# Optimization experiments

Measured on AMD Instinct MI355X. Metric: run time of the kernel, lower is better.

## Reference

```python
import jax, jax.numpy as jnp
import numpy as np
import math

L = 16.0
DT = 1.0
TAU = 10.0
THRESHOLD = 1.0
ALPHA = 0.01
DECAY = math.exp(-DT / TAU)

@jax.custom_vjp
def multibit_spike(x):
    # forward: floor(x) clipped to [0, L]
    return jnp.clip(jnp.floor(x), 0.0, L)

def _spike_fwd(x):
    return multibit_spike(x), x

def _spike_bwd(x, g):
    dist = jnp.abs(x - jnp.round(x))
    scale = jnp.clip(1.0 - 2.0 * dist, 0.0, 1.0)
    in_range = ((x >= 0.0) & (x <= L + 1.0)).astype(g.dtype)
    return (g * in_range * scale,)

multibit_spike.defvjp(_spike_fwd, _spike_bwd)

def setup_inputs() -> dict:
    key = jax.random.key(0)
    k_x, k_w = jax.random.split(key)
    B, T, IN, H = 16, 2048, 512, 512
    # SNN-aware init: std = 0.5*threshold / (sqrt(fan_in)*0.3)
    std = 0.5 * THRESHOLD / (math.sqrt(IN) * 0.3)
    x = jax.random.normal(k_x, (B, T, IN), dtype=jnp.float32)
    W = jax.random.normal(k_w, (H, IN), dtype=jnp.float32) * std
    b = jnp.zeros((H,), dtype=jnp.float32)
    return {"x": x, "W": W, "b": b}

def reference(x, W, b):
    B, T, _ = x.shape
    Hd = W.shape[0]
    # batched linear projection of the whole sequence (compute-heavy GEMM)
    h = jnp.einsum('bti,hi->bth', x, W) + b  # [B, T, H]
    v0 = jnp.zeros((B, Hd), dtype=x.dtype)
    theta0 = jnp.full((B, Hd), THRESHOLD, dtype=x.dtype)

    def step(carry, i_t):
        v, theta = carry
        v = v * DECAY + i_t
        clamp_limit = L * theta * 2.0
        v = jnp.clip(v, -clamp_limit, clamp_limit)
        spike = multibit_spike(v / theta)
        v = v - spike * theta
        theta = theta + ALPHA * spike - ALPHA * (theta - THRESHOLD)
        return (v, theta), spike

    (v_f, theta_f), spikes_tbh = jax.lax.scan(step, (v0, theta0), jnp.swapaxes(h, 0, 1))
    spikes = jnp.swapaxes(spikes_tbh, 0, 1)  # [B, T, H]
    return spikes, v_f, theta_f
```

## Files before the change

kernel.cpp:

```cpp
#include <hip/hip_runtime.h>

#define B_  16
#define T_  2048
#define IN_ 512
#define H_  512
#define M_  (B_ * T_)

#define BM 128
#define BN 128
#define BK 16
#define LDT (BM + 4)

static __device__ __forceinline__ float4 ld4(const float* p) {
    return *reinterpret_cast<const float4*>(p);
}

__global__ __launch_bounds__(256)
void gemm_xwT(const float* __restrict__ X, const float* __restrict__ W,
              const float* __restrict__ bias, float* __restrict__ Hout) {
    __shared__ float As[BK][LDT];
    __shared__ float Bs[BK][LDT];

    const int tid = threadIdx.x;
    const int m0  = blockIdx.x * BM;
    const int n0  = blockIdx.y * BN;

    const int tx = tid & 15;
    const int ty = tid >> 4;

    const int row = tid >> 2;
    const int kph = (tid & 3) * 4;

    const float* pa0 = X + (size_t)(m0 + row) * IN_ + kph;
    const float* pa1 = pa0 + (size_t)64 * IN_;
    const float* pb0 = W + (size_t)(n0 + row) * IN_ + kph;
    const float* pb1 = pb0 + (size_t)64 * IN_;

    float4 ra0 = ld4(pa0), ra1 = ld4(pa1), rb0 = ld4(pb0), rb1 = ld4(pb1);

    float acc[8][8];
#pragma unroll
    for (int i = 0; i < 8; ++i)
#pragma unroll
        for (int j = 0; j < 8; ++j) acc[i][j] = 0.0f;

    for (int k0 = 0; k0 < IN_; k0 += BK) {
        As[kph + 0][row]      = ra0.x;  As[kph + 1][row]      = ra0.y;
        As[kph + 2][row]      = ra0.z;  As[kph + 3][row]      = ra0.w;
        As[kph + 0][row + 64] = ra1.x;  As[kph + 1][row + 64] = ra1.y;
        As[kph + 2][row + 64] = ra1.z;  As[kph + 3][row + 64] = ra1.w;
        Bs[kph + 0][row]      = rb0.x;  Bs[kph + 1][row]      = rb0.y;
        Bs[kph + 2][row]      = rb0.z;  Bs[kph + 3][row]      = rb0.w;
        Bs[kph + 0][row + 64] = rb1.x;  Bs[kph + 1][row + 64] = rb1.y;
        Bs[kph + 2][row + 64] = rb1.z;  Bs[kph + 3][row + 64] = rb1.w;
        __syncthreads();

        if (k0 + BK < IN_) {
            ra0 = ld4(pa0 + k0 + BK);  ra1 = ld4(pa1 + k0 + BK);
            rb0 = ld4(pb0 + k0 + BK);  rb1 = ld4(pb1 + k0 + BK);
        }

#pragma unroll
        for (int k = 0; k < BK; ++k) {
            float4 av0 = ld4(&As[k][ty * 4]);
            float4 av1 = ld4(&As[k][ty * 4 + 64]);
            float4 bv0 = ld4(&Bs[k][tx * 4]);
            float4 bv1 = ld4(&Bs[k][tx * 4 + 64]);
            const float am[8] = {av0.x, av0.y, av0.z, av0.w,
                                 av1.x, av1.y, av1.z, av1.w};
            const float bn8[8] = {bv0.x, bv0.y, bv0.z, bv0.w,
                                  bv1.x, bv1.y, bv1.z, bv1.w};
#pragma unroll
            for (int i = 0; i < 8; ++i)
#pragma unroll
                for (int j = 0; j < 8; ++j)
                    acc[i][j] = fmaf(am[i], bn8[j], acc[i][j]);
        }
        __syncthreads();
    }

    float4 bb0 = ld4(&bias[n0 + tx * 4]);
    float4 bb1 = ld4(&bias[n0 + tx * 4 + 64]);
#pragma unroll
    for (int i = 0; i < 8; ++i) {
        const int r = m0 + ((i < 4) ? (ty * 4 + i) : (64 + ty * 4 + (i - 4)));
        float4 o0, o1;
        o0.x = acc[i][0] + bb0.x;  o0.y = acc[i][1] + bb0.y;
        o0.z = acc[i][2] + bb0.z;  o0.w = acc[i][3] + bb0.w;
        o1.x = acc[i][4] + bb1.x;  o1.y = acc[i][5] + bb1.y;
        o1.z = acc[i][6] + bb1.z;  o1.w = acc[i][7] + bb1.w;
        *reinterpret_cast<float4*>(&Hout[(size_t)r * H_ + n0 + tx * 4])      = o0;
        *reinterpret_cast<float4*>(&Hout[(size_t)r * H_ + n0 + tx * 4 + 64]) = o1;
    }
}

#define PF 32

__global__ __launch_bounds__(256)
void gif_scan(const float* __restrict__ Hbuf, float* __restrict__ spikes,
              float* __restrict__ vout, float* __restrict__ thout) {
    const int gid = blockIdx.x * 256 + threadIdx.x;
    const int b = gid >> 9;
    const int h = gid & 511;

    const float* ip = Hbuf   + (size_t)b * T_ * H_ + h;
    float*       sp = spikes + (size_t)b * T_ * H_ + h;

    const float DECAY_F = 0.9048374180359595f;
    const float ALPHA_F = 0.01f;

    float buf[PF];
#pragma unroll
    for (int j = 0; j < PF; ++j) buf[j] = ip[(size_t)j * H_];

    float v = 0.0f, theta = 1.0f;
    for (int t0 = 0; t0 < T_; t0 += PF) {
        float nbuf[PF];
        const int tnx = t0 + PF;
        if (tnx < T_) {
#pragma unroll
            for (int j = 0; j < PF; ++j) nbuf[j] = ip[(size_t)(tnx + j) * H_];
        }
#pragma unroll
        for (int j = 0; j < PF; ++j) {
            float cur = buf[j];
            v = v * DECAY_F + cur;
            float cl = 32.0f * theta;
            v = fminf(fmaxf(v, -cl), cl);

            float r0 = __builtin_amdgcn_rcpf(theta);
            float e0 = fmaf(-theta, r0, 1.0f);
            float r1 = fmaf(r0, e0, r0);
            float e1 = fmaf(-theta, r1, 1.0f);
            float r2 = fmaf(r1, e1, r1);
            float q0 = v * r2;
            float er = fmaf(-theta, q0, v);
            float q  = fmaf(er, r2, q0);

            float s = floorf(q);
            s = fminf(fmaxf(s, 0.0f), 16.0f);
            v = v - s * theta;
            theta = theta + ALPHA_F * s - ALPHA_F * (theta - 1.0f);
            sp[(size_t)(t0 + j) * H_] = s;
        }
#pragma unroll
        for (int j = 0; j < PF; ++j) buf[j] = nbuf[j];
    }
    vout[gid]  = v;
    thout[gid] = theta;
}

extern "C" void kernel_launch(void* const* d_in, const int* in_sizes, int n_in,
                              void* d_out, int out_size, void* d_ws, size_t ws_size,
                              hipStream_t stream) {
    const float* x    = (const float*)d_in[0];
    const float* W    = (const float*)d_in[1];
    const float* bias = (const float*)d_in[2];

    float* out    = (float*)d_out;
    float* spikes = out;
    float* v_f    = out + (size_t)M_ * H_;
    float* th_f   = v_f + (size_t)B_ * H_;

    float* hbuf   = (float*)d_ws;

    dim3 grid(M_ / BM, H_ / BN);
    gemm_xwT<<<grid, 256, 0, stream>>>(x, W, bias, hbuf);
    gif_scan<<<(B_ * H_) / 256, 256, 0, stream>>>(hbuf, spikes, v_f, th_f);
}
```

Baseline: 408.5 us.

## Ping-pong buffer scan prefetch, use med3 clamps, one Newton step, 64-thread blocks

```diff
diff --git a/kernel.cpp b/kernel.cpp
--- a/kernel.cpp
+++ b/kernel.cpp
@@ -94,57 +94,63 @@
     }
 }
 
-#define PF 32
+#define SPF 32
 
-__global__ __launch_bounds__(256)
+__device__ __forceinline__
+void scan_steps(const float* __restrict__ buf, float* __restrict__ sp,
+                int tb, float& v, float& theta) {
+    const float DECAY_F = 0.9048374180359595f;
+    const float ALPHA_F = 0.01f;
+#pragma unroll
+    for (int j = 0; j < SPF; ++j) {
+        float cur = buf[j];
+        v = v * DECAY_F + cur;
+        float cl = 32.0f * theta;
+        v = __builtin_amdgcn_fmed3f(v, -cl, cl);
+
+        float r0 = __builtin_amdgcn_rcpf(theta);
+        float e0 = fmaf(-theta, r0, 1.0f);
+        float r1 = fmaf(r0, e0, r0);
+        float q0 = v * r1;
+        float er = fmaf(-theta, q0, v);
+        float q  = fmaf(er, r1, q0);
+
+        float s = floorf(q);
+        s = __builtin_amdgcn_fmed3f(s, 0.0f, 16.0f);
+        v = v - s * theta;
+        theta = theta + ALPHA_F * s - ALPHA_F * (theta - 1.0f);
+        sp[(size_t)(tb + j) * H_] = s;
+    }
+}
+
+__global__ __launch_bounds__(64)
 void gif_scan(const float* __restrict__ Hbuf, float* __restrict__ spikes,
               float* __restrict__ vout, float* __restrict__ thout) {
-    const int gid = blockIdx.x * 256 + threadIdx.x;
+    const int gid = blockIdx.x * 64 + threadIdx.x;
     const int b = gid >> 9;
     const int h = gid & 511;
 
     const float* ip = Hbuf   + (size_t)b * T_ * H_ + h;
     float*       sp = spikes + (size_t)b * T_ * H_ + h;
 
-    const float DECAY_F = 0.9048374180359595f;
-    const float ALPHA_F = 0.01f;
-
-    float buf[PF];
+    float bufA[SPF], bufB[SPF];
 #pragma unroll
-    for (int j = 0; j < PF; ++j) buf[j] = ip[(size_t)j * H_];
+    for (int j = 0; j < SPF; ++j) bufA[j] = ip[(size_t)j * H_];
 
     float v = 0.0f, theta = 1.0f;
-    for (int t0 = 0; t0 < T_; t0 += PF) {
-        float nbuf[PF];
-        const int tnx = t0 + PF;
-        if (tnx < T_) {
+    for (int t0 = 0; t0 < T_; t0 += 2 * SPF) {
 #pragma unroll
-            for (int j = 0; j < PF; ++j) nbuf[j] = ip[(size_t)(tnx + j) * H_];
+        for (int j = 0; j < SPF; ++j) bufB[j] = ip[(size_t)(t0 + SPF + j) * H_];
+        asm volatile("" ::: "memory");
+        scan_steps(bufA, sp, t0, v, theta);
+
+        if (t0 + 2 * SPF < T_) {
+#pragma unroll
+            for (int j = 0; j < SPF; ++j)
+                bufA[j] = ip[(size_t)(t0 + 2 * SPF + j) * H_];
         }
-#pragma unroll
-        for (int j = 0; j < PF; ++j) {
-            float cur = buf[j];
-            v = v * DECAY_F + cur;
-            float cl = 32.0f * theta;
-            v = fminf(fmaxf(v, -cl), cl);
-
-            float r0 = __builtin_amdgcn_rcpf(theta);
-            float e0 = fmaf(-theta, r0, 1.0f);
-            float r1 = fmaf(r0, e0, r0);
-            float e1 = fmaf(-theta, r1, 1.0f);
-            float r2 = fmaf(r1, e1, r1);
-            float q0 = v * r2;
-            float er = fmaf(-theta, q0, v);
-            float q  = fmaf(er, r2, q0);
-
-            float s = floorf(q);
-            s = fminf(fmaxf(s, 0.0f), 16.0f);
-            v = v - s * theta;
-            theta = theta + ALPHA_F * s - ALPHA_F * (theta - 1.0f);
-            sp[(size_t)(t0 + j) * H_] = s;
-        }
-#pragma unroll
-        for (int j = 0; j < PF; ++j) buf[j] = nbuf[j];
+        asm volatile("" ::: "memory");
+        scan_steps(bufB, sp, t0 + SPF, v, theta);
     }
     vout[gid]  = v;
     thout[gid] = theta;
@@ -166,5 +172,5 @@
 
     dim3 grid(M_ / BM, H_ / BN);
     gemm_xwT<<<grid, 256, 0, stream>>>(x, W, bias, hbuf);
-    gif_scan<<<(B_ * H_) / 256, 256, 0, stream>>>(hbuf, spikes, v_f, th_f);
+    gif_scan<<<(B_ * H_) / 64, 64, 0, stream>>>(hbuf, spikes, v_f, th_f);
 }
```

Measured after the change: 370.2 us. -9.4%, faster.
